# Kernel tuning notes

Hardware: AMD Instinct MI355X
Metric: run time of the kernel (lower is better)

## Reference

```python
import jax, jax.numpy as jnp
import numpy as np

G = 13            # grid_size
A = 5             # num_anchors
C = 36            # num_classes
OBJ_SCALE = 5.0
NOOBJ_SCALE = 1.0
CLASS_SCALE = 1.0
COORD_SCALE = 1.0
ANCHORS = jnp.array([[1.08, 1.19], [3.42, 4.41], [6.63, 11.38], [9.42, 5.11], [16.62, 10.52]], dtype=jnp.float32)


def setup_inputs() -> dict:
    key = jax.random.key(0)
    k1, k2, k3 = jax.random.split(key, 3)
    B, T = 1024, 30
    predictions = jax.random.normal(k1, (B, A * (5 + C), G, G), dtype=jnp.float32)
    # x,y,w,h normalized to (0,1); class id in [0,C) stored as float in channel 4
    xywh = jax.random.uniform(k2, (B, T, 4), dtype=jnp.float32, minval=1e-3, maxval=0.999)
    cls = jax.random.randint(k3, (B, T, 1), 0, C).astype(jnp.float32)
    target = jnp.concatenate([xywh, cls], axis=-1)
    return {"predictions": predictions, "target": target}


def build_targets(target):
    # target: [B, T, 5]  (x, y, w, h, class), x/y/w/h in [0,1)
    B, T, _ = target.shape
    valid = jnp.sum(target, axis=-1) != 0                      # [B, T]
    gx = target[..., 0] * G
    gy = target[..., 1] * G
    gw = target[..., 2] * G
    gh = target[..., 3] * G
    gi = gx.astype(jnp.int32)                                  # int() truncation (values >= 0)
    gj = gy.astype(jnp.int32)
    # anchor IoU for boxes centered at origin: inter = min(w)*min(h)
    aw = ANCHORS[:, 0]                                          # [A]
    ah = ANCHORS[:, 1]
    inter = jnp.minimum(gw[..., None], aw) * jnp.minimum(gh[..., None], ah)   # [B,T,A]
    union = (gw * gh)[..., None] + aw * ah - inter
    iou = inter / (union + 1e-16)
    best_n = jnp.argmax(iou, axis=-1)                           # [B, T] first-max, matches torch loop
    baw = ANCHORS[best_n, 0]
    bah = ANCHORS[best_n, 1]
    tx = gx - gi.astype(gx.dtype)
    ty = gy - gj.astype(gy.dtype)
    tw = jnp.log(gw / baw + 1e-16)
    th = jnp.log(gh / bah + 1e-16)
    cls_idx = target[..., 4].astype(jnp.int32)                  # [B, T]

    N = B * A * G * G
    b_idx = jnp.arange(B, dtype=jnp.int32)[:, None]             # [B,1] -> broadcast to [B,T]
    flat = ((b_idx * A + best_n.astype(jnp.int32)) * G + gj) * G + gi   # [B,T]
    flat = jnp.where(valid, flat, N)                            # out-of-bounds -> dropped
    flat = flat.reshape(-1)                                     # [B*T]

    conf_mask = jnp.full((N,), NOOBJ_SCALE, dtype=jnp.float32).at[flat].set(OBJ_SCALE, mode="drop")
    coord_mask = jnp.zeros((N, 4), dtype=jnp.float32).at[flat].set(1.0, mode="drop")
    class_mask = jnp.zeros((N, C), dtype=jnp.float32).at[flat].set(CLASS_SCALE, mode="drop")
    tconf = jnp.zeros((N,), dtype=jnp.float32).at[flat].set(1.0, mode="drop")
    tcoord_vals = jnp.stack([tx, ty, tw, th], axis=-1).reshape(-1, 4)
    tcoord = jnp.zeros((N, 4), dtype=jnp.float32).at[flat].set(tcoord_vals, mode="drop")
    tclass = jnp.zeros((N, C), dtype=jnp.float32).at[flat, cls_idx.reshape(-1)].set(1.0, mode="drop")

    shp = (B, A, G, G)
    return (coord_mask.reshape(shp + (4,)), conf_mask.reshape(shp), class_mask.reshape(shp + (C,)),
            tcoord.reshape(shp + (4,)), tconf.reshape(shp), tclass.reshape(shp + (C,)))


def reference(predictions, target):
    B = predictions.shape[0]
    p = predictions.reshape(B, A, 5 + C, G, G).transpose(0, 1, 3, 4, 2)   # [B,A,G,G,5+C]
    coord_mask, conf_mask, class_mask, tcoord, tconf, tclass = build_targets(target)
    pred_coord = p[..., 1:5]
    pred_conf = jax.nn.sigmoid(p[..., 0])
    pred_class = p[..., 5:]
    loss_coord = COORD_SCALE * jnp.sum((pred_coord * coord_mask - tcoord * coord_mask) ** 2) / B
    loss_conf = jnp.sum((pred_conf * conf_mask - tconf * conf_mask) ** 2) / B
    labels = jnp.argmax(tclass.reshape(-1, C), axis=1)
    logp = jax.nn.log_softmax(pred_class.reshape(-1, C), axis=-1)
    loss_class = CLASS_SCALE * (-jnp.take_along_axis(logp, labels[:, None], axis=1).sum()) / B
    total_loss = loss_coord + loss_conf + loss_class
    return (total_loss, loss_coord, loss_conf, loss_class)
```

## Files before the change

### kernel.cpp

```cpp
#include <hip/hip_runtime.h>

#define GQ 13
#define AQ 5
#define CQ 36
#define TQ 30
#define CH (5 + CQ)
#define GG (GQ * GQ)
#define CELLS (AQ * GG)
#define BLOCK 896
#define NWAVES (BLOCK / 64)


__global__ __launch_bounds__(BLOCK) void yolo_main(
    const float* __restrict__ pred,
    const float* __restrict__ target,
    double* __restrict__ acc)
{
    __shared__ int   s_cell[TQ];
    __shared__ float s_tc[TQ][4];
    __shared__ int   s_cls[TQ];
    __shared__ float s_red[3][NWAVES];

    const int b   = blockIdx.x;
    const int tid = threadIdx.x;

    if (tid < TQ) {
        const float* tg = target + ((size_t)b * TQ + tid) * 5;
        float x = tg[0], y = tg[1], w = tg[2], h = tg[3], c5 = tg[4];
        bool valid = (x + y + w + h + c5) != 0.0f;
        float gx = x * GQ, gy = y * GQ, gw = w * GQ, gh = h * GQ;
        int gi = (int)gx, gj = (int)gy;
        const float AW[5] = {1.08f, 3.42f, 6.63f, 9.42f, 16.62f};
        const float AH[5] = {1.19f, 4.41f, 11.38f, 5.11f, 10.52f};
        float best = -1.0f; int bn = 0;
        #pragma unroll
        for (int a = 0; a < AQ; a++) {
            float inter = fminf(gw, AW[a]) * fminf(gh, AH[a]);
            float un    = gw * gh + AW[a] * AH[a] - inter;
            float iou   = inter / (un + 1e-16f);
            if (iou > best) { best = iou; bn = a; }
        }
        s_cell[tid]  = valid ? ((bn * GQ + gj) * GQ + gi) : -1;
        s_tc[tid][0] = gx - (float)gi;
        s_tc[tid][1] = gy - (float)gj;
        s_tc[tid][2] = logf(gw / AW[bn] + 1e-16f);
        s_tc[tid][3] = logf(gh / AH[bn] + 1e-16f);
        s_cls[tid]   = (int)c5;
    }
    __syncthreads();

    float lcoord = 0.0f, lconf = 0.0f, lclass = 0.0f;
    if (tid < CELLS) {
        int a   = tid / GG;
        int rem = tid - a * GG;
        const float* base = pred + ((size_t)(b * AQ + a) * CH) * GG + rem;

        bool obj = false; int minc = CQ;
        float tx = 0.f, ty = 0.f, tw = 0.f, th = 0.f;
        #pragma unroll
        for (int t = 0; t < TQ; t++) {
            if (s_cell[t] == tid) {
                obj = true;
                tx = s_tc[t][0]; ty = s_tc[t][1];
                tw = s_tc[t][2]; th = s_tc[t][3];
                minc = min(minc, s_cls[t]);
            }
        }
        int label = obj ? minc : 0;

        float p0  = base[0];
        float sig = 1.0f / (1.0f + __expf(-p0));
        if (obj) {
            float d = 5.0f * (sig - 1.0f);
            lconf = d * d;
            float d1 = base[1 * GG] - tx;
            float d2 = base[2 * GG] - ty;
            float d3 = base[3 * GG] - tw;
            float d4 = base[4 * GG] - th;
            lcoord = d1 * d1 + d2 * d2 + d3 * d3 + d4 * d4;
        } else {
            lconf = sig * sig;
        }

        float v[CQ];
        float m = -3.0e38f, vl = 0.0f;
        #pragma unroll
        for (int c = 0; c < CQ; c++) {
            v[c] = base[(size_t)(5 + c) * GG];
            m = fmaxf(m, v[c]);
            vl = (c == label) ? v[c] : vl;
        }
        float sum = 0.0f;
        #pragma unroll
        for (int c = 0; c < CQ; c++) sum += __expf(v[c] - m);
        lclass = -(vl - m - __logf(sum));
    }

    #pragma unroll
    for (int off = 32; off > 0; off >>= 1) {
        lcoord += __shfl_down(lcoord, off, 64);
        lconf  += __shfl_down(lconf,  off, 64);
        lclass += __shfl_down(lclass, off, 64);
    }
    int wv = tid >> 6, ln = tid & 63;
    if (ln == 0) { s_red[0][wv] = lcoord; s_red[1][wv] = lconf; s_red[2][wv] = lclass; }
    __syncthreads();
    if (tid == 0) {
        float a0 = 0.f, a1 = 0.f, a2 = 0.f;
        #pragma unroll
        for (int w = 0; w < NWAVES; w++) { a0 += s_red[0][w]; a1 += s_red[1][w]; a2 += s_red[2][w]; }
        atomicAdd(acc + 0, (double)a0);
        atomicAdd(acc + 1, (double)a1);
        atomicAdd(acc + 2, (double)a2);
    }
}

__global__ void yolo_final(const double* __restrict__ acc, float* __restrict__ out, float Bf)
{
    double inv = 1.0 / (double)Bf;
    float fcoord = (float)(acc[0] * inv);
    float fconf  = (float)(acc[1] * inv);
    float fclass = (float)(acc[2] * inv);
    out[0] = fcoord + fconf + fclass;
    out[1] = fcoord;
    out[2] = fconf;
    out[3] = fclass;
}

extern "C" void kernel_launch(void* const* d_in, const int* in_sizes, int n_in,
                              void* d_out, int out_size, void* d_ws, size_t ws_size,
                              hipStream_t stream)
{
    const float* pred   = (const float*)d_in[0];
    const float* target = (const float*)d_in[1];
    float*  out = (float*)d_out;
    double* acc = (double*)d_ws;

    int B = in_sizes[0] / (AQ * CH * GG);

    hipMemsetAsync(d_ws, 0, 3 * sizeof(double), stream);
    yolo_main<<<B, BLOCK, 0, stream>>>(pred, target, acc);
    yolo_final<<<1, 1, 0, stream>>>(acc, out, (float)B);
}
```

Measured before the change: 223.1 us.

## Vectorize per-thread cell processing with float4 loads and fuse finalization

Each thread now handles four adjacent grid cells, loading them with float4 reads. The last thread per anchor overlaps the tail and masks out the duplicate cells. Per-target assignment moves into a shared cell-info table built serially by one thread, so each cell no longer scans all 30 targets. Softmax drops the max subtraction, which risks overflow for large logits. The finalize kernel is removed in favour of float atomics straight into the output, trading double-precision accumulation for fewer launches.

After: 247.6 us. 11.0% more time.

```diff
diff --git a/kernel.cpp b/kernel.cpp
--- a/kernel.cpp
+++ b/kernel.cpp
@@ -7,22 +7,26 @@
 #define CH (5 + CQ)
 #define GG (GQ * GQ)
 #define CELLS (AQ * GG)
-#define BLOCK 896
-#define NWAVES (BLOCK / 64)
+#define JPP 43
+#define ACT (AQ * JPP)
+#define BLOCK 256
 
 
-__global__ __launch_bounds__(BLOCK) void yolo_main(
+__global__ __launch_bounds__(BLOCK) void yolo_fused(
     const float* __restrict__ pred,
     const float* __restrict__ target,
-    double* __restrict__ acc)
+    float* __restrict__ out, float invB)
 {
+    __shared__ int   s_info[CELLS];
     __shared__ int   s_cell[TQ];
     __shared__ float s_tc[TQ][4];
     __shared__ int   s_cls[TQ];
-    __shared__ float s_red[3][NWAVES];
+    __shared__ float s_red[3][BLOCK / 64];
 
     const int b   = blockIdx.x;
     const int tid = threadIdx.x;
+
+    for (int i = tid; i < CELLS; i += BLOCK) s_info[i] = 0;
 
     if (tid < TQ) {
         const float* tg = target + ((size_t)b * TQ + tid) * 5;
@@ -43,57 +47,83 @@
         s_cell[tid]  = valid ? ((bn * GQ + gj) * GQ + gi) : -1;
         s_tc[tid][0] = gx - (float)gi;
         s_tc[tid][1] = gy - (float)gj;
-        s_tc[tid][2] = logf(gw / AW[bn] + 1e-16f);
-        s_tc[tid][3] = logf(gh / AH[bn] + 1e-16f);
+        s_tc[tid][2] = __logf(gw / AW[bn] + 1e-16f);
+        s_tc[tid][3] = __logf(gh / AH[bn] + 1e-16f);
         s_cls[tid]   = (int)c5;
     }
     __syncthreads();
 
-    float lcoord = 0.0f, lconf = 0.0f, lclass = 0.0f;
-    if (tid < CELLS) {
-        int a   = tid / GG;
-        int rem = tid - a * GG;
-        const float* base = pred + ((size_t)(b * AQ + a) * CH) * GG + rem;
-
-        bool obj = false; int minc = CQ;
-        float tx = 0.f, ty = 0.f, tw = 0.f, th = 0.f;
-        #pragma unroll
+    if (tid == 0) {
+        #pragma unroll 1
         for (int t = 0; t < TQ; t++) {
-            if (s_cell[t] == tid) {
-                obj = true;
-                tx = s_tc[t][0]; ty = s_tc[t][1];
-                tw = s_tc[t][2]; th = s_tc[t][3];
-                minc = min(minc, s_cls[t]);
+            int c = s_cell[t];
+            if (c >= 0) {
+                int lab = s_cls[t];
+                int old = s_info[c];
+                if (old) lab = min(lab, old & 0xff);
+                s_info[c] = 0x40000000 | (t << 8) | lab;
             }
         }
-        int label = obj ? minc : 0;
+    }
+    __syncthreads();
 
-        float p0  = base[0];
-        float sig = 1.0f / (1.0f + __expf(-p0));
-        if (obj) {
-            float d = 5.0f * (sig - 1.0f);
-            lconf = d * d;
-            float d1 = base[1 * GG] - tx;
-            float d2 = base[2 * GG] - ty;
-            float d3 = base[3 * GG] - tw;
-            float d4 = base[4 * GG] - th;
-            lcoord = d1 * d1 + d2 * d2 + d3 * d3 + d4 * d4;
-        } else {
-            lconf = sig * sig;
+    float lcoord = 0.0f, lconf = 0.0f, lclass = 0.0f;
+    if (tid < ACT) {
+        int a = tid / JPP;
+        int j = tid - a * JPP;
+        bool tail = (j == JPP - 1);
+        int rem0 = tail ? (GG - 4) : (j * 4);
+        const float* base = pred + (size_t)((b * AQ + a) * CH) * GG + rem0;
+        int cell0 = a * GG + rem0;
+
+        float actm[4];
+        #pragma unroll
+        for (int e = 0; e < 4; e++) actm[e] = (!tail || e == 3) ? 1.0f : 0.0f;
+
+        int info[4];
+        #pragma unroll
+        for (int e = 0; e < 4; e++) info[e] = s_info[cell0 + e];
+
+        float4 pc; __builtin_memcpy(&pc, base, 16);
+        float cf[4] = {pc.x, pc.y, pc.z, pc.w};
+        #pragma unroll
+        for (int e = 0; e < 4; e++) {
+            float sig = 1.0f / (1.0f + __expf(-cf[e]));
+            float d = info[e] ? 5.0f * (sig - 1.0f) : sig;
+            lconf += actm[e] * d * d;
         }
 
-        float v[CQ];
-        float m = -3.0e38f, vl = 0.0f;
+        #pragma unroll
+        for (int e = 0; e < 4; e++) {
+            if (info[e] && actm[e] != 0.0f) {
+                int t = (info[e] >> 8) & 0xff;
+                float d1 = base[1 * GG + e] - s_tc[t][0];
+                float d2 = base[2 * GG + e] - s_tc[t][1];
+                float d3 = base[3 * GG + e] - s_tc[t][2];
+                float d4 = base[4 * GG + e] - s_tc[t][3];
+                lcoord += d1 * d1 + d2 * d2 + d3 * d3 + d4 * d4;
+            }
+        }
+
+        int lab[4];
+        #pragma unroll
+        for (int e = 0; e < 4; e++) lab[e] = info[e] & 0xff;
+        float sum[4] = {0.f, 0.f, 0.f, 0.f};
+        float vl[4]  = {0.f, 0.f, 0.f, 0.f};
+        const float* cbase = base + 5 * GG;
         #pragma unroll
         for (int c = 0; c < CQ; c++) {
-            v[c] = base[(size_t)(5 + c) * GG];
-            m = fmaxf(m, v[c]);
-            vl = (c == label) ? v[c] : vl;
+            float4 v; __builtin_memcpy(&v, cbase + (size_t)c * GG, 16);
+            float vv[4] = {v.x, v.y, v.z, v.w};
+            #pragma unroll
+            for (int e = 0; e < 4; e++) {
+                sum[e] += __expf(vv[e]);
+                vl[e] = (c == lab[e]) ? vv[e] : vl[e];
+            }
         }
-        float sum = 0.0f;
         #pragma unroll
-        for (int c = 0; c < CQ; c++) sum += __expf(v[c] - m);
-        lclass = -(vl - m - __logf(sum));
+        for (int e = 0; e < 4; e++)
+            lclass += actm[e] * (__logf(sum[e]) - vl[e]);
     }
 
     #pragma unroll
@@ -108,23 +138,15 @@
     if (tid == 0) {
         float a0 = 0.f, a1 = 0.f, a2 = 0.f;
         #pragma unroll
-        for (int w = 0; w < NWAVES; w++) { a0 += s_red[0][w]; a1 += s_red[1][w]; a2 += s_red[2][w]; }
-        atomicAdd(acc + 0, (double)a0);
-        atomicAdd(acc + 1, (double)a1);
-        atomicAdd(acc + 2, (double)a2);
+        for (int w = 0; w < BLOCK / 64; w++) {
+            a0 += s_red[0][w]; a1 += s_red[1][w]; a2 += s_red[2][w];
+        }
+        a0 *= invB; a1 *= invB; a2 *= invB;
+        atomicAdd(out + 0, a0 + a1 + a2);
+        atomicAdd(out + 1, a0);
+        atomicAdd(out + 2, a1);
+        atomicAdd(out + 3, a2);
     }
-}
-
-__global__ void yolo_final(const double* __restrict__ acc, float* __restrict__ out, float Bf)
-{
-    double inv = 1.0 / (double)Bf;
-    float fcoord = (float)(acc[0] * inv);
-    float fconf  = (float)(acc[1] * inv);
-    float fclass = (float)(acc[2] * inv);
-    out[0] = fcoord + fconf + fclass;
-    out[1] = fcoord;
-    out[2] = fconf;
-    out[3] = fclass;
 }
 
 extern "C" void kernel_launch(void* const* d_in, const int* in_sizes, int n_in,
@@ -133,12 +155,10 @@
 {
     const float* pred   = (const float*)d_in[0];
     const float* target = (const float*)d_in[1];
-    float*  out = (float*)d_out;
-    double* acc = (double*)d_ws;
+    float* out = (float*)d_out;
 
     int B = in_sizes[0] / (AQ * CH * GG);
 
-    hipMemsetAsync(d_ws, 0, 3 * sizeof(double), stream);
-    yolo_main<<<B, BLOCK, 0, stream>>>(pred, target, acc);
-    yolo_final<<<1, 1, 0, stream>>>(acc, out, (float)B);
+    hipMemsetAsync(d_out, 0, 4 * sizeof(float), stream);
+    yolo_fused<<<B, BLOCK, 0, stream>>>(pred, target, out, 1.0f / (float)B);
 }
```
